# Kernel tuning notes

Measured on AMD Instinct MI355X. Metric: run time of the kernel, lower is better.

Reference implementation:

```python
import jax, jax.numpy as jnp
import numpy as np

NX, NY = 4096, 4096


def setup_inputs() -> dict:
    key = jax.random.key(0)
    k1, k2 = jax.random.split(key)
    u_main = jax.random.normal(k1, (NX, NY), dtype=jnp.float32)
    u_coupled = jax.random.normal(k2, (NX, NY), dtype=jnp.float32)
    D_eff = jnp.array([0.05], dtype=jnp.float32)
    dirichlet_val = jnp.array([1.0, 0.0, 1.0, 0.0], dtype=jnp.float32)
    stencil = jnp.array([1.0, -1.0], dtype=jnp.float32)  # fixed [1,-1] stencil
    return {
        "u_main": u_main,
        "u_coupled": u_coupled,
        "D_eff": D_eff,
        "dirichlet_val": dirichlet_val,
        "stencil": stencil,
        "t": 1,
    }


def reference(u_main, u_coupled, D_eff, dirichlet_val, stencil, t):
    # Flux_Kernels.forward with Dirichlet BCs on all four boundaries and
    # is_retardation_a_func=False (ret_inv = ones), so u_coupled and t are unused.
    D = D_eff[0]
    s0, s1 = stencil[0], stencil[1]
    ret = jnp.ones_like(u_main)  # ret_inv when no retardation function

    # left (x- direction): boundary row 0, neighbors rows 1..Nx-1
    left_bound = ((s0 * dirichlet_val[0] + s1 * u_main[0, :]) * D * ret[0, :])[None, :]
    left_nb = (s0 * u_main[:-1, :] + s1 * u_main[1:, :]) * D * ret[1:, :]
    left_flux = jnp.concatenate([left_bound, left_nb], axis=0)

    # right (x+ direction): neighbors rows 0..Nx-2, boundary row Nx-1
    right_bound = ((s0 * dirichlet_val[1] + s1 * u_main[-1, :]) * D * ret[-1, :])[None, :]
    right_nb = (s0 * u_main[1:, :] + s1 * u_main[:-1, :]) * D * ret[:-1, :]
    right_flux = jnp.concatenate([right_nb, right_bound], axis=0)

    # top (y- direction): boundary col 0, neighbors cols 1..Ny-1
    top_bound = ((s0 * dirichlet_val[2] + s1 * u_main[:, 0]) * D * ret[:, 0])[:, None]
    top_nb = (s0 * u_main[:, :-1] + s1 * u_main[:, 1:]) * D * ret[:, 1:]
    top_flux = jnp.concatenate([top_bound, top_nb], axis=1)

    # bottom (y+ direction): neighbors cols 0..Ny-2, boundary col Ny-1
    bottom_bound = ((s0 * dirichlet_val[3] + s1 * u_main[:, -1]) * D * ret[:, -1])[:, None]
    bottom_nb = (s0 * u_main[:, 1:] + s1 * u_main[:, :-1]) * D * ret[:, :-1]
    bottom_flux = jnp.concatenate([bottom_nb, bottom_bound], axis=1)

    return left_flux + right_flux + top_flux + bottom_flux
```

## Files before the change

kernel.cpp:

```cpp
#include <hip/hip_runtime.h>


#define NX 4096
#define NY 4096
#define ROWS 16
#define NBUF 8

__global__ __launch_bounds__(256) void flux_stencil_kernel(
    const float* __restrict__ u,
    const float* __restrict__ D_eff,
    const float* __restrict__ dv,
    const float* __restrict__ st,
    float* __restrict__ out)
{
    const float D  = D_eff[0];
    const float s0 = st[0];
    const float s1 = st[1];
    const float k1 = D * s0;
    const float k4 = 4.0f * D * s1;
    const float dvUp = dv[0], dvDn = dv[1], dvL = dv[2], dvR = dv[3];

    const int hw   = blockIdx.x;
    const int x    = hw & 7;
    const int band = ((x & 1) << 7) + (hw >> 3);
    const int cg   = x >> 1;
    const int w    = threadIdx.x >> 6;
    const int lane = threadIdx.x & 63;
    const int j    = cg * 1024 + w * 256 + lane * 4;
    const int i0   = band * ROWS;

    const float* rowp = u   + (size_t)i0 * NY + j;
    float*       outp = out + (size_t)i0 * NY + j;

    float4 buf[NBUF];
    buf[0] = (i0 == 0) ? make_float4(dvUp, dvUp, dvUp, dvUp)
                       : *reinterpret_cast<const float4*>(rowp - NY);
    #pragma unroll
    for (int k = 0; k < 6; ++k)
        buf[k + 1] = *reinterpret_cast<const float4*>(rowp + k * NY);

    float le[ROWS], re[ROWS];
    const bool lEdge = (j == 0);
    const bool rEdge = (j + 4 == NY);
    if (lane == 0) {
        #pragma unroll
        for (int k = 0; k < ROWS; ++k)
            le[k] = lEdge ? dvL : rowp[k * NY - 1];
    }
    if (lane == 63) {
        #pragma unroll
        for (int k = 0; k < ROWS; ++k)
            re[k] = rEdge ? dvR : rowp[k * NY + 4];
    }

    #pragma unroll
    for (int r = 0; r < ROWS; ++r) {
        if (r <= ROWS - 6) {
            const int row = i0 + r + 6;
            buf[(r + 7) % NBUF] =
                (row >= NX) ? make_float4(dvDn, dvDn, dvDn, dvDn)
                            : *reinterpret_cast<const float4*>(rowp + (r + 6) * NY);
        }

        const float4 up = buf[r % NBUF];
        const float4 cc = buf[(r + 1) % NBUF];
        const float4 dn = buf[(r + 2) % NBUF];

        float lft = __shfl_up(cc.w, 1);
        float rgt = __shfl_down(cc.x, 1);
        if (lane == 0)  lft = le[r];
        if (lane == 63) rgt = re[r];

        float4 o;
        o.x = k1 * (up.x + dn.x + lft  + cc.y) + k4 * cc.x;
        o.y = k1 * (up.y + dn.y + cc.x + cc.z) + k4 * cc.y;
        o.z = k1 * (up.z + dn.z + cc.y + cc.w) + k4 * cc.z;
        o.w = k1 * (up.w + dn.w + cc.z + rgt ) + k4 * cc.w;
        *reinterpret_cast<float4*>(outp + r * NY) = o;
    }
}

extern "C" void kernel_launch(void* const* d_in, const int* in_sizes, int n_in,
                              void* d_out, int out_size, void* d_ws, size_t ws_size,
                              hipStream_t stream) {
    const float* u_main    = (const float*)d_in[0];
    const float* D_eff     = (const float*)d_in[2];
    const float* dirichlet = (const float*)d_in[3];
    const float* stencil   = (const float*)d_in[4];
    float* outp = (float*)d_out;

    const int grid  = 1024;
    const int block = 256;

    flux_stencil_kernel<<<grid, block, 0, stream>>>(u_main, D_eff, dirichlet, stencil, outp);
}
```

Baseline: 27.08 us.

## Replace lane shuffles with overlapping unaligned float4 loads for horizontal neighbors

Each thread now issues two unaligned float4 loads per row, offset by -1 and +1 columns, and rebuilds its center values and left/right neighbors from them. This removes the cross-lane shuffles and the per-lane edge loads done by lanes 0 and 63. The prefetch depth changes to 4 rows ahead, and edge rows use clamped addresses with Dirichlet values substituted afterwards. The cost is about twice the load instructions, which mostly hit the same cache lines, plus unaligned accesses and higher register pressure from the full-slot arrays.

```diff
diff --git a/kernel.cpp b/kernel.cpp
--- a/kernel.cpp
+++ b/kernel.cpp
@@ -4,7 +4,11 @@
 #define NX 4096
 #define NY 4096
 #define ROWS 16
-#define NBUF 8
+#define PF 4
+#define SLOTS (ROWS + 2)
+
+typedef float float4v __attribute__((ext_vector_type(4)));
+typedef float float4a __attribute__((ext_vector_type(4), aligned(4)));
 
 __global__ __launch_bounds__(256) void flux_stencil_kernel(
     const float* __restrict__ u,
@@ -29,55 +33,70 @@
     const int j    = cg * 1024 + w * 256 + lane * 4;
     const int i0   = band * ROWS;
 
-    const float* rowp = u   + (size_t)i0 * NY + j;
+    const bool fL = (j == 0);
+    const bool fR = (j + 4 == NY);
+    const int  aO = fL ? 0 : -1;
+    const int  bO = fR ? 0 : 1;
+    const bool topEdge = (i0 == 0);
+    const bool botEdge = (i0 + ROWS == NX);
+
+    const float* base = u   + (size_t)i0 * NY + j;
     float*       outp = out + (size_t)i0 * NY + j;
 
-    float4 buf[NBUF];
-    buf[0] = (i0 == 0) ? make_float4(dvUp, dvUp, dvUp, dvUp)
-                       : *reinterpret_cast<const float4*>(rowp - NY);
-    #pragma unroll
-    for (int k = 0; k < 6; ++k)
-        buf[k + 1] = *reinterpret_cast<const float4*>(rowp + k * NY);
+    float4v A[SLOTS], B[SLOTS];
+    float4v cc[SLOTS];
+    float   lf[SLOTS], rg[SLOTS];
 
-    float le[ROWS], re[ROWS];
-    const bool lEdge = (j == 0);
-    const bool rEdge = (j + 4 == NY);
-    if (lane == 0) {
-        #pragma unroll
-        for (int k = 0; k < ROWS; ++k)
-            le[k] = lEdge ? dvL : rowp[k * NY - 1];
+    #define ISSUE(k)                                                           \
+    {                                                                          \
+        int rr = (k) - 1;                                                      \
+        if ((k) == 0 && topEdge)          rr = 0;            \
+        if ((k) == ROWS + 1 && botEdge)   rr = ROWS - 1;     \
+        const float* p = base + (ptrdiff_t)rr * NY;                            \
+        A[k] = *reinterpret_cast<const float4a*>(p + aO);                      \
+        B[k] = *reinterpret_cast<const float4a*>(p + bO);                      \
     }
-    if (lane == 63) {
-        #pragma unroll
-        for (int k = 0; k < ROWS; ++k)
-            re[k] = rEdge ? dvR : rowp[k * NY + 4];
+
+    #define RECON(k)                                                           \
+    {                                                                          \
+        const float4v a = A[k], b = B[k];                                      \
+        float4v c;                                                             \
+        c.x = fL ? a.x : a.y;                                                  \
+        c.y = fL ? a.y : a.z;                                                  \
+        c.z = fL ? a.z : a.w;                                                  \
+        c.w = fR ? b.w : b.z;                                                  \
+        lf[k] = fL ? dvL : a.x;                                                \
+        rg[k] = fR ? dvR : b.w;                                                \
+        if ((k) == 0 && topEdge)        { c.x = dvUp; c.y = dvUp; c.z = dvUp; c.w = dvUp; } \
+        if ((k) == ROWS + 1 && botEdge) { c.x = dvDn; c.y = dvDn; c.z = dvDn; c.w = dvDn; } \
+        cc[k] = c;                                                             \
+    }
+
+    #define STORE(k)                                                           \
+    {                                                                          \
+        const float4v up = cc[(k) - 2], c = cc[(k) - 1], dn = cc[k];           \
+        const float l = lf[(k) - 1], r = rg[(k) - 1];                          \
+        float4v o;                                                             \
+        o.x = k1 * (up.x + dn.x + l   + c.y) + k4 * c.x;                       \
+        o.y = k1 * (up.y + dn.y + c.x + c.z) + k4 * c.y;                       \
+        o.z = k1 * (up.z + dn.z + c.y + c.w) + k4 * c.z;                       \
+        o.w = k1 * (up.w + dn.w + c.z + r  ) + k4 * c.w;                       \
+        *reinterpret_cast<float4v*>(outp + (size_t)((k) - 2) * NY) = o;        \
     }
 
     #pragma unroll
-    for (int r = 0; r < ROWS; ++r) {
-        if (r <= ROWS - 6) {
-            const int row = i0 + r + 6;
-            buf[(r + 7) % NBUF] =
-                (row >= NX) ? make_float4(dvDn, dvDn, dvDn, dvDn)
-                            : *reinterpret_cast<const float4*>(rowp + (r + 6) * NY);
-        }
+    for (int k = 0; k < PF; ++k) ISSUE(k)
 
-        const float4 up = buf[r % NBUF];
-        const float4 cc = buf[(r + 1) % NBUF];
-        const float4 dn = buf[(r + 2) % NBUF];
+    #pragma unroll
+    for (int k = 0; k < SLOTS; ++k) {
+        if (k + PF < SLOTS) ISSUE(k + PF)
+        RECON(k)
+        if (k >= 2) STORE(k)
+    }
 
-        float lft = __shfl_up(cc.w, 1);
-        float rgt = __shfl_down(cc.x, 1);
-        if (lane == 0)  lft = le[r];
-        if (lane == 63) rgt = re[r];
-
-        float4 o;
-        o.x = k1 * (up.x + dn.x + lft  + cc.y) + k4 * cc.x;
-        o.y = k1 * (up.y + dn.y + cc.x + cc.z) + k4 * cc.y;
-        o.z = k1 * (up.z + dn.z + cc.y + cc.w) + k4 * cc.z;
-        o.w = k1 * (up.w + dn.w + cc.z + rgt ) + k4 * cc.w;
-        *reinterpret_cast<float4*>(outp + r * NY) = o;
-    }
+    #undef ISSUE
+    #undef RECON
+    #undef STORE
 }
 
 extern "C" void kernel_launch(void* const* d_in, const int* in_sizes, int n_in,
```

New measurement: 26.15 us. 3.4% less time.
